# Optimization experiments

Hardware: AMD Instinct MI355X
Metric: run time of the kernel (lower is better)

The kernel has to match this reference:

```python
import jax, jax.numpy as jnp
import numpy as np

H = 400           # size_hidden_layer
F = 128           # nFeatures
S = 128           # seq_len
B = 256           # batch
K_OUT = 5         # size_output_layer


def lstm_layer(x, kernel, bias):
    """TF LSTMCell semantics: gates i, j, f, o; forget_bias=1.0.
    x: [B,S,D], kernel: [D+H, 4H], bias: [4H] -> returns [B,S,H]."""
    b = x.shape[0]
    h0 = jnp.zeros((b, H), x.dtype)
    c0 = jnp.zeros((b, H), x.dtype)
    xT = jnp.swapaxes(x, 0, 1)  # [S,B,D]

    def step(carry, xt):
        h, c = carry
        z = jnp.concatenate([xt, h], axis=1) @ kernel + bias  # [B,4H]
        i, j, f, o = jnp.split(z, 4, axis=1)
        c_new = c * jax.nn.sigmoid(f + 1.0) + jax.nn.sigmoid(i) * jnp.tanh(j)
        h_new = jnp.tanh(c_new) * jax.nn.sigmoid(o)
        return (h_new, c_new), h_new

    _, ys = jax.lax.scan(step, (h0, c0), xT)
    return jnp.swapaxes(ys, 0, 1)  # [B,S,H]


def setup_inputs() -> dict:
    key = jax.random.key(0)
    ks = jax.random.split(key, 8)
    x = jax.random.normal(ks[0], (B, S, F), dtype=jnp.float32)
    # LSTM kernels (glorot-ish small init); layer 0 input F, others H
    k0 = 0.05 * jax.random.normal(ks[1], (F + H, 4 * H), dtype=jnp.float32)
    k1 = 0.05 * jax.random.normal(ks[2], (H + H, 4 * H), dtype=jnp.float32)
    k2 = 0.05 * jax.random.normal(ks[3], (H + H, 4 * H), dtype=jnp.float32)
    b0 = jnp.zeros((4 * H,), jnp.float32)
    b1 = jnp.zeros((4 * H,), jnp.float32)
    b2 = jnp.zeros((4 * H,), jnp.float32)
    # Output heads: truncated_normal(stddev=0.01) weights, 0.1 biases
    w_lg = 0.01 * jax.random.normal(ks[4], (H, 1), dtype=jnp.float32)
    b_lg = jnp.full((1,), 0.1, jnp.float32)
    w_sm2 = 0.01 * jax.random.normal(ks[5], (H, 2), dtype=jnp.float32)
    b_sm2 = jnp.full((2,), 0.1, jnp.float32)
    w = 0.01 * jax.random.normal(ks[6], (H, K_OUT), dtype=jnp.float32)
    b = jnp.full((K_OUT,), 0.1, jnp.float32)
    return {"x": x, "k0": k0, "b0": b0, "k1": k1, "b1": b1, "k2": k2,
            "b2": b2, "w_lg": w_lg, "b_lg": b_lg, "w_sm2": w_sm2,
            "b_sm2": b_sm2, "w": w, "b": b}


def reference(x, k0, b0, k1, b1, k2, b2, w_lg, b_lg, w_sm2, b_sm2, w, b):
    h = lstm_layer(x, k0, b0)
    h = lstm_layer(h, k1, b1)
    h = lstm_layer(h, k2, b2)          # [B,S,H]
    pred_mc = jax.nn.sigmoid(h @ w_lg + b_lg)            # [B,S,1]
    pred_md = jax.nn.softmax(h @ w_sm2 + b_sm2, axis=-1)  # [B,S,2]
    pred_mg = jax.nn.softmax(h @ w + b, axis=-1)          # [B,S,5]
    return jnp.concatenate([pred_mc, pred_md, pred_mg], axis=-1)  # [B,S,8]
```

## Files before the change

kernel.cpp:

```cpp
#include <hip/hip_runtime.h>
#include <hip/hip_bf16.h>


typedef __attribute__((ext_vector_type(8))) short bf16x8;
typedef __attribute__((ext_vector_type(4))) float f32x4;

#define S_LEN 128
#define HID   400
#define NCOL  1600
#define NCB   25
#define KT_REC 13
#define WS_NEEDED 173358080ull

__device__ __forceinline__ f32x4 mfma16(bf16x8 a, bf16x8 b, f32x4 c) {
  return __builtin_amdgcn_mfma_f32_16x16x32_bf16(a, b, c, 0, 0, 0);
}
__device__ __forceinline__ void gll16(const void* g, void* l) {
  __builtin_amdgcn_global_load_lds(
      (const __attribute__((address_space(1))) void*)g,
      (__attribute__((address_space(3))) void*)l, 16, 0, 0);
}
__device__ __forceinline__ float bf2f(__hip_bfloat16 h) { return __bfloat162float(h); }
__device__ __forceinline__ __hip_bfloat16 f2bf(float f) { return __float2bfloat16(f); }
__device__ __forceinline__ float sigm(float x) { return 1.f / (1.f + __expf(-x)); }
__device__ __forceinline__ float tanh_fast(float x) { return 1.f - 2.f / (__expf(2.f * x) + 1.f); }

__global__ __launch_bounds__(256) void cvt_x_kernel(const float* __restrict__ x,
                                                    __hip_bfloat16* __restrict__ xbf) {
  const int i = blockIdx.x * 256 + threadIdx.x;
  float4 v = ((const float4*)x)[i];
  ushort4 u;
  u.x = __builtin_bit_cast(unsigned short, f2bf(v.x));
  u.y = __builtin_bit_cast(unsigned short, f2bf(v.y));
  u.z = __builtin_bit_cast(unsigned short, f2bf(v.z));
  u.w = __builtin_bit_cast(unsigned short, f2bf(v.w));
  ((ushort4*)xbf)[i] = u;
}

__global__ __launch_bounds__(256) void prep_gemm_frag(
    const float* __restrict__ K0, const float* __restrict__ K1,
    const float* __restrict__ K2, __hip_bfloat16* __restrict__ wfrag) {
  const int total = 3200 * 512;
  for (int e = blockIdx.x * 256 + threadIdx.x; e < total; e += gridDim.x * 256) {
    const int ch = e >> 9, r = e & 511;
    const int c16 = r & 15, j = (r >> 4) & 7, kg = r >> 7;
    const float* W; int Kv, chL;
    if (ch < 400)       { W = K0; Kv = 128; chL = ch; }
    else if (ch < 1800) { W = K1; Kv = 400; chL = ch - 400; }
    else                { W = K2; Kv = 400; chL = ch - 1800; }
    const int kt = chL / 100, nt = chL - kt * 100;
    const int k = kt * 32 + kg * 8 + j;
    const float v = (k < Kv) ? W[(long)k * NCOL + nt * 16 + c16] : 0.f;
    wfrag[(ch << 9) + ((kg * 16 + c16) << 3) + j] = f2bf(v);
  }
}

__global__ __launch_bounds__(256) void prep_rec_frag(
    const float* __restrict__ K0, const float* __restrict__ K1,
    const float* __restrict__ K2, __hip_bfloat16* __restrict__ rfrag) {
  const int perL = 25 * 52 * 512;
  const int total = 3 * perL;
  for (int e = blockIdx.x * 256 + threadIdx.x; e < total; e += gridDim.x * 256) {
    const int l = e / perL, eL = e - l * perL;
    const int ch = eL >> 9, r = eL & 511;
    const int c16 = r & 15, j = (r >> 4) & 7, kg = r >> 7;
    const int cb = ch / 52, rem = ch - cb * 52;
    const int kt = rem >> 2, w = rem & 3;
    const int k = kt * 32 + kg * 8 + j;
    const int col = w * 400 + cb * 16 + c16;
    const float* W = (l == 0) ? K0 : ((l == 1) ? K1 : K2);
    const int D = (l == 0) ? 128 : 400;
    const float v = (k < HID) ? W[(long)(D + k) * NCOL + col] : 0.f;
    rfrag[(long)l * perL + (ch << 9) + ((kg * 16 + c16) << 3) + j] = f2bf(v);
  }
}

__global__ __launch_bounds__(256) void gemm_kernel(
    const __hip_bfloat16* __restrict__ A, int lda, int kIters,
    const __hip_bfloat16* __restrict__ wfrag, const float* __restrict__ bias,
    __hip_bfloat16* __restrict__ C) {
  __shared__ uint4 lds4[32 * 64];
  char* lds = (char*)lds4;
  const int tid = threadIdx.x;
  const int wave = tid >> 6, lane = tid & 63;
  const int wm = wave >> 1, wn = wave & 1;
  const int m0 = blockIdx.x << 7, n0 = blockIdx.y << 7;

  f32x4 acc[4][4];
#pragma unroll
  for (int i = 0; i < 4; ++i)
#pragma unroll
    for (int j = 0; j < 4; ++j) acc[i][j] = (f32x4){0.f, 0.f, 0.f, 0.f};

  for (int it = 0; it < kIters; ++it) {
    const int k0 = it << 6;
#pragma unroll
    for (int q = 0; q < 8; ++q) {
      const int id = wave * 8 + q;
      char* dst = lds + (id << 10);
      if (id < 16) {
        const int kk = id >> 3, mt = id & 7;
        const int m = m0 + mt * 16 + (lane & 15);
        int k = k0 + kk * 32 + ((lane >> 4) << 3);
        if (k + 8 > lda) k = 0;
        gll16((const char*)A + (((long)m * lda + k) << 1), dst);
      } else {
        const int kk = (id >> 3) & 1, nt = id & 7;
        const int ktg = (it << 1) + kk;
        int ntg = (n0 >> 4) + nt;
        if (ntg > 99) ntg = 99;
        gll16((const char*)wfrag + ((((ktg * 100 + ntg) << 6) + lane) << 4), dst);
      }
    }
    asm volatile("s_waitcnt vmcnt(0)" ::: "memory");
    __syncthreads();
#pragma unroll
    for (int kk = 0; kk < 2; ++kk) {
      bf16x8 af[4], bfr[4];
#pragma unroll
      for (int i = 0; i < 4; ++i) {
        af[i]  = *(const bf16x8*)(lds + ((kk * 8 + wm * 4 + i) << 10) + (lane << 4));
        bfr[i] = *(const bf16x8*)(lds + ((16 + kk * 8 + wn * 4 + i) << 10) + (lane << 4));
      }
#pragma unroll
      for (int i = 0; i < 4; ++i)
#pragma unroll
        for (int j = 0; j < 4; ++j) acc[i][j] = mfma16(af[i], bfr[j], acc[i][j]);
    }
    __syncthreads();
  }
  const int rowbase = m0 + wm * 64 + ((lane >> 4) << 2);
  const int colbase = n0 + wn * 64 + (lane & 15);
#pragma unroll
  for (int j = 0; j < 4; ++j) {
    const int col = colbase + j * 16;
    if (col < NCOL) {
      const float bs = bias[col];
#pragma unroll
      for (int i = 0; i < 4; ++i) {
        const int row = rowbase + i * 16;
#pragma unroll
        for (int r = 0; r < 4; ++r)
          C[(long)(row + r) * NCOL + col] = f2bf(acc[i][j][r] + bs);
      }
    }
  }
}

__global__ __launch_bounds__(256) void rec_kernel(
    const __hip_bfloat16* __restrict__ rfrag,
    const __hip_bfloat16* __restrict__ preZ,
    __hip_bfloat16* __restrict__ Hout,
    __hip_bfloat16* __restrict__ hbuf,
    unsigned* __restrict__ flags) {
  __shared__ uint4 AldsV[26 * 64];
  __shared__ float zlds[4 * 32 * 16];
  char* Alds = (char*)AldsV;

  const int g = blockIdx.x & 7;
  const int cB = blockIdx.x >> 3;
  const int tid = threadIdx.x;
  const int wave = tid >> 6, lane = tid & 63;

  bf16x8 breg[KT_REC];
#pragma unroll
  for (int kt = 0; kt < KT_REC; ++kt) {
    uint4 u = ((const uint4*)rfrag)[((cB * KT_REC + kt) * 4 + wave) * 64 + lane];
    breg[kt] = __builtin_bit_cast(bf16x8, u);
  }

  float cst0 = 0.f, cst1 = 0.f;
  const int u16 = tid & 15, r0 = tid >> 4;

  for (int t = 0; t < S_LEN; ++t) {
    const int p = t & 1;

    const int b0r = g * 32 + r0;
    const long pz0 = ((long)b0r * S_LEN + t) * NCOL + cB * 16 + u16;
    const long pz1 = ((long)(b0r + 16) * S_LEN + t) * NCOL + cB * 16 + u16;
    const float pzi0 = bf2f(preZ[pz0]);
    const float pzj0 = bf2f(preZ[pz0 + 400]);
    const float pzf0 = bf2f(preZ[pz0 + 800]);
    const float pzo0 = bf2f(preZ[pz0 + 1200]);
    const float pzi1 = bf2f(preZ[pz1]);
    const float pzj1 = bf2f(preZ[pz1 + 400]);
    const float pzf1 = bf2f(preZ[pz1 + 800]);
    const float pzo1 = bf2f(preZ[pz1 + 1200]);

    for (int cc = wave; cc < 26; cc += 4) {
      const int kt = cc >> 1, mt = cc & 1;
      const int b = g * 32 + mt * 16 + (lane & 15);
      int k = kt * 32 + ((lane >> 4) << 3);
      if (k >= HID) k = 0;
      gll16((const char*)hbuf + (((p * 256 + b) * HID + k) << 1), Alds + (cc << 10));
    }
    asm volatile("s_waitcnt vmcnt(0)" ::: "memory");
    __syncthreads();

    f32x4 acc0 = (f32x4){0.f, 0.f, 0.f, 0.f}, acc1 = acc0;
#pragma unroll
    for (int kt = 0; kt < KT_REC; ++kt) {
      bf16x8 a0 = *(const bf16x8*)(Alds + ((kt * 2 + 0) << 10) + (lane << 4));
      bf16x8 a1 = *(const bf16x8*)(Alds + ((kt * 2 + 1) << 10) + (lane << 4));
      acc0 = mfma16(a0, breg[kt], acc0);
      acc1 = mfma16(a1, breg[kt], acc1);
    }
    {
      const int colz = lane & 15, rb = (lane >> 4) << 2;
#pragma unroll
      for (int r = 0; r < 4; ++r) {
        zlds[(wave * 32 + rb + r) * 16 + colz] = acc0[r];
        zlds[(wave * 32 + rb + r + 16) * 16 + colz] = acc1[r];
      }
    }
    __syncthreads();

#pragma unroll
    for (int half = 0; half < 2; ++half) {
      const int row = r0 + half * 16;
      const int b = g * 32 + row;
      const long mrow = (long)b * S_LEN + t;
      const float zi = zlds[(0 * 32 + row) * 16 + u16] + (half ? pzi1 : pzi0);
      const float zj = zlds[(1 * 32 + row) * 16 + u16] + (half ? pzj1 : pzj0);
      const float zf = zlds[(2 * 32 + row) * 16 + u16] + (half ? pzf1 : pzf0) + 1.f;
      const float zo = zlds[(3 * 32 + row) * 16 + u16] + (half ? pzo1 : pzo0);
      float c_old = half ? cst1 : cst0;
      const float cn = c_old * sigm(zf) + sigm(zi) * tanh_fast(zj);
      if (half) cst1 = cn; else cst0 = cn;
      const float hv = tanh_fast(cn) * sigm(zo);
      const __hip_bfloat16 hb16 = f2bf(hv);
      Hout[mrow * HID + cB * 16 + u16] = hb16;
      hbuf[((1 - p) * 256 + b) * HID + cB * 16 + u16] = hb16;
    }
    __threadfence();
    __syncthreads();
    if (t == S_LEN - 1) break;

    const unsigned tgt = (unsigned)(t + 1);
    if (tid == 0)
      __hip_atomic_store(&flags[g * 32 + cB], tgt, __ATOMIC_RELEASE,
                         __HIP_MEMORY_SCOPE_AGENT);
    if (wave == 0) {
      while (true) {
        unsigned v = tgt;
        if (lane < NCB)
          v = __hip_atomic_load(&flags[g * 32 + lane], __ATOMIC_ACQUIRE,
                                __HIP_MEMORY_SCOPE_AGENT);
        if (__all((int)(v >= tgt))) break;
        __builtin_amdgcn_s_sleep(2);
      }
    }
    __syncthreads();
    __threadfence();
  }
}

__global__ __launch_bounds__(256) void heads_kernel(
    const __hip_bfloat16* __restrict__ H, const float* __restrict__ wlg,
    const float* __restrict__ blg, const float* __restrict__ wsm2,
    const float* __restrict__ bsm2, const float* __restrict__ w5,
    const float* __restrict__ b5, float* __restrict__ out) {
  __shared__ float wc[8][400];
  const int tid = threadIdx.x;
  for (int e = tid; e < 3200; e += 256) {
    const int cc = e / 400, k = e - cc * 400;
    float v;
    if (cc == 0) v = wlg[k];
    else if (cc <= 2) v = wsm2[k * 2 + (cc - 1)];
    else v = w5[k * 5 + (cc - 3)];
    wc[cc][k] = v;
  }
  __syncthreads();
  const int wave = tid >> 6, lane = tid & 63;
  const int row = blockIdx.x * 4 + wave;
  const __hip_bfloat16* hrow = H + (long)row * HID;
  float pacc[8] = {0.f, 0.f, 0.f, 0.f, 0.f, 0.f, 0.f, 0.f};
  for (int k = lane; k < HID; k += 64) {
    const float hv = bf2f(hrow[k]);
#pragma unroll
    for (int cc = 0; cc < 8; ++cc) pacc[cc] += hv * wc[cc][k];
  }
#pragma unroll
  for (int cc = 0; cc < 8; ++cc)
    for (int off = 32; off > 0; off >>= 1)
      pacc[cc] += __shfl_xor(pacc[cc], off, 64);
  if (lane == 0) {
    const float o0 = sigm(pacc[0] + blg[0]);
    const float z1 = pacc[1] + bsm2[0], z2 = pacc[2] + bsm2[1];
    const float mm = fmaxf(z1, z2);
    const float e1 = __expf(z1 - mm), e2 = __expf(z2 - mm);
    const float inv2 = 1.f / (e1 + e2);
    float z5[5], m5 = -1e30f;
#pragma unroll
    for (int c = 0; c < 5; ++c) { z5[c] = pacc[3 + c] + b5[c]; m5 = fmaxf(m5, z5[c]); }
    float es[5], s5 = 0.f;
#pragma unroll
    for (int c = 0; c < 5; ++c) { es[c] = __expf(z5[c] - m5); s5 += es[c]; }
    const float inv5 = 1.f / s5;
    float4* op = (float4*)(out + (long)row * 8);
    op[0] = make_float4(o0, e1 * inv2, e2 * inv2, es[0] * inv5);
    op[1] = make_float4(es[1] * inv5, es[2] * inv5, es[3] * inv5, es[4] * inv5);
  }
}

extern "C" void kernel_launch(void* const* d_in, const int* in_sizes, int n_in,
                              void* d_out, int out_size, void* d_ws, size_t ws_size,
                              hipStream_t stream) {
  (void)in_sizes; (void)n_in; (void)out_size;
  if (ws_size < WS_NEEDED) return;

  const float* x    = (const float*)d_in[0];
  const float* K0   = (const float*)d_in[1];
  const float* B0   = (const float*)d_in[2];
  const float* K1   = (const float*)d_in[3];
  const float* B1   = (const float*)d_in[4];
  const float* K2   = (const float*)d_in[5];
  const float* B2   = (const float*)d_in[6];
  const float* wlg  = (const float*)d_in[7];
  const float* blg  = (const float*)d_in[8];
  const float* wsm2 = (const float*)d_in[9];
  const float* bsm2 = (const float*)d_in[10];
  const float* w5   = (const float*)d_in[11];
  const float* b5   = (const float*)d_in[12];
  float* out = (float*)d_out;
  char* ws = (char*)d_ws;

  __hip_bfloat16* xbf   = (__hip_bfloat16*)(ws + 0);
  __hip_bfloat16* HA    = (__hip_bfloat16*)(ws + 8388608);
  __hip_bfloat16* HB    = (__hip_bfloat16*)(ws + 34603008);
  __hip_bfloat16* preZ  = (__hip_bfloat16*)(ws + 60817408);
  __hip_bfloat16* hbuf  = (__hip_bfloat16*)(ws + 165675008);
  __hip_bfloat16* wfrag = (__hip_bfloat16*)(ws + 166084608);
  __hip_bfloat16* rfrag = (__hip_bfloat16*)(ws + 169361408);
  unsigned* flags       = (unsigned*)(ws + 173355008);

  hipMemsetAsync(flags, 0, 3072, stream);
  hipMemsetAsync(hbuf, 0, 204800, stream);
  cvt_x_kernel<<<4096, 256, 0, stream>>>(x, xbf);
  prep_gemm_frag<<<2048, 256, 0, stream>>>(K0, K1, K2, wfrag);
  prep_rec_frag<<<2048, 256, 0, stream>>>(K0, K1, K2, rfrag);

  gemm_kernel<<<dim3(256, 13), 256, 0, stream>>>(xbf, 128, 2, wfrag, B0, preZ);
  rec_kernel<<<200, 256, 0, stream>>>(rfrag, preZ, HA, hbuf, flags);

  hipMemsetAsync(hbuf, 0, 204800, stream);
  gemm_kernel<<<dim3(256, 13), 256, 0, stream>>>(HA, 400, 7, wfrag + 204800, B1, preZ);
  rec_kernel<<<200, 256, 0, stream>>>(rfrag + 665600, preZ, HB, hbuf, flags + 256);

  hipMemsetAsync(hbuf, 0, 204800, stream);
  gemm_kernel<<<dim3(256, 13), 256, 0, stream>>>(HB, 400, 7, wfrag + 921600, B2, preZ);
  rec_kernel<<<200, 256, 0, stream>>>(rfrag + 1331200, preZ, HA, hbuf, flags + 512);

  heads_kernel<<<8192, 256, 0, stream>>>(HA, wlg, blg, wsm2, bsm2, w5, b5, out);
}
```

Measured before the change: 13.43 ms.

## Replace multi-block flag-synced recurrence with per-batch-group single-block LSTM kernel

The recurrent step now runs as 16 independent blocks of 832 threads, each owning 16 batch rows and all 400 hidden units. This removes the cross-block atomic flag barriers and global h exchange. Recurrent weights are held in registers across 13 waves, h is ping-ponged in LDS, and next-step preZ is prefetched into LDS with async global-to-LDS loads. The cost is that only 16 CUs are used, with a very high register load per wave, so each block carries much more serial MFMA work per step.

```diff
diff --git a/kernel.cpp b/kernel.cpp
--- a/kernel.cpp
+++ b/kernel.cpp
@@ -8,9 +8,7 @@
 #define S_LEN 128
 #define HID   400
 #define NCOL  1600
-#define NCB   25
-#define KT_REC 13
-#define WS_NEEDED 173358080ull
+#define WS_NEEDED 173105152ull
 
 __device__ __forceinline__ f32x4 mfma16(bf16x8 a, bf16x8 b, f32x4 c) {
   return __builtin_amdgcn_mfma_f32_16x16x32_bf16(a, b, c, 0, 0, 0);
@@ -24,6 +22,10 @@
 __device__ __forceinline__ __hip_bfloat16 f2bf(float f) { return __float2bfloat16(f); }
 __device__ __forceinline__ float sigm(float x) { return 1.f / (1.f + __expf(-x)); }
 __device__ __forceinline__ float tanh_fast(float x) { return 1.f - 2.f / (__expf(2.f * x) + 1.f); }
+__device__ __forceinline__ float ldbf(const char* p) {
+  const unsigned short u = *(const unsigned short*)p;
+  return __builtin_bit_cast(float, (unsigned)u << 16);
+}
 
 __global__ __launch_bounds__(256) void cvt_x_kernel(const float* __restrict__ x,
                                                     __hip_bfloat16* __restrict__ xbf) {
@@ -58,20 +60,22 @@
 __global__ __launch_bounds__(256) void prep_rec_frag(
     const float* __restrict__ K0, const float* __restrict__ K1,
     const float* __restrict__ K2, __hip_bfloat16* __restrict__ rfrag) {
-  const int perL = 25 * 52 * 512;
+  const int perL = 1352 * 512;
   const int total = 3 * perL;
   for (int e = blockIdx.x * 256 + threadIdx.x; e < total; e += gridDim.x * 256) {
     const int l = e / perL, eL = e - l * perL;
     const int ch = eL >> 9, r = eL & 511;
-    const int c16 = r & 15, j = (r >> 4) & 7, kg = r >> 7;
-    const int cb = ch / 52, rem = ch - cb * 52;
-    const int kt = rem >> 2, w = rem & 3;
-    const int k = kt * 32 + kg * 8 + j;
-    const int col = w * 400 + cb * 16 + c16;
+    const int lane = r >> 3, j = r & 7;
+    const int kt = ch % 13;
+    int c2 = ch / 13;
+    const int ut = c2 & 1; c2 >>= 1;
+    const int q = c2 & 3;  const int w = c2 >> 2;
+    const int unit = w * 32 + ut * 16 + (lane & 15);
+    const int k = kt * 32 + ((lane >> 4) << 3) + j;
     const float* W = (l == 0) ? K0 : ((l == 1) ? K1 : K2);
     const int D = (l == 0) ? 128 : 400;
-    const float v = (k < HID) ? W[(long)(D + k) * NCOL + col] : 0.f;
-    rfrag[(long)l * perL + (ch << 9) + ((kg * 16 + c16) << 3) + j] = f2bf(v);
+    const float v = (k < HID && unit < HID) ? W[(long)(D + k) * NCOL + q * 400 + unit] : 0.f;
+    rfrag[(long)l * perL + (ch << 9) + (lane << 3) + j] = f2bf(v);
   }
 }
 
@@ -147,111 +151,120 @@
   }
 }
 
-__global__ __launch_bounds__(256) void rec_kernel(
-    const __hip_bfloat16* __restrict__ rfrag,
+__device__ __forceinline__ void stage_pz(const __hip_bfloat16* __restrict__ preZ,
+                                         int G, int t, char* dstbase,
+                                         int tid, int wv) {
+#pragma unroll
+  for (int it = 0; it < 4; ++it) {
+    const int s = it * 832 + tid;
+    if (s < 3200) {
+      const int row = s / 200;
+      const int off = s - row * 200;
+      const long gb = ((long)((G * 16 + row) * 128 + t)) * 3200 + (long)off * 16;
+      gll16((const char*)preZ + gb, dstbase + (it * 832 + (wv << 6)) * 16);
+    }
+  }
+}
+
+__global__ __launch_bounds__(832, 1) void rec2_kernel(
+    const __hip_bfloat16* __restrict__ rfragL,
     const __hip_bfloat16* __restrict__ preZ,
-    __hip_bfloat16* __restrict__ Hout,
-    __hip_bfloat16* __restrict__ hbuf,
-    unsigned* __restrict__ flags) {
-  __shared__ uint4 AldsV[26 * 64];
-  __shared__ float zlds[4 * 32 * 16];
-  char* Alds = (char*)AldsV;
-
-  const int g = blockIdx.x & 7;
-  const int cB = blockIdx.x >> 3;
+    __hip_bfloat16* __restrict__ Hout) {
+  __shared__ __attribute__((aligned(16))) char smem[129536];
+  char* const pz0 = smem;
+  char* const pz1 = smem + 51200;
+  char* const h0  = smem + 102400;
+  char* const h1  = smem + 102400 + 13568;
+
   const int tid = threadIdx.x;
-  const int wave = tid >> 6, lane = tid & 63;
-
-  bf16x8 breg[KT_REC];
-#pragma unroll
-  for (int kt = 0; kt < KT_REC; ++kt) {
-    uint4 u = ((const uint4*)rfrag)[((cB * KT_REC + kt) * 4 + wave) * 64 + lane];
-    breg[kt] = __builtin_bit_cast(bf16x8, u);
-  }
-
-  float cst0 = 0.f, cst1 = 0.f;
-  const int u16 = tid & 15, r0 = tid >> 4;
+  const int wv = tid >> 6, lane = tid & 63;
+  const int l15 = lane & 15, l4 = lane >> 4;
+  const int G = blockIdx.x;
+
+  for (int s = tid; s < 6784; s += 832) ((unsigned*)h0)[s] = 0;
+
+  stage_pz(preZ, G, 0, pz0, tid, wv);
+
+  bf16x8 Bw[4][2][13];
+  {
+    const uint4* rp = (const uint4*)rfragL;
+#pragma unroll
+    for (int q = 0; q < 4; ++q)
+#pragma unroll
+      for (int ut = 0; ut < 2; ++ut)
+#pragma unroll
+        for (int kt = 0; kt < 13; ++kt)
+          Bw[q][ut][kt] = __builtin_bit_cast(
+              bf16x8, rp[((((wv * 4 + q) * 2 + ut) * 13) + kt) * 64 + lane]);
+  }
+
+  float cs[2][4];
+#pragma unroll
+  for (int ut = 0; ut < 2; ++ut)
+#pragma unroll
+    for (int r = 0; r < 4; ++r) cs[ut][r] = 0.f;
+
+  const int hrow = l15 * 424 * 2;
+  __syncthreads();
 
   for (int t = 0; t < S_LEN; ++t) {
     const int p = t & 1;
-
-    const int b0r = g * 32 + r0;
-    const long pz0 = ((long)b0r * S_LEN + t) * NCOL + cB * 16 + u16;
-    const long pz1 = ((long)(b0r + 16) * S_LEN + t) * NCOL + cB * 16 + u16;
-    const float pzi0 = bf2f(preZ[pz0]);
-    const float pzj0 = bf2f(preZ[pz0 + 400]);
-    const float pzf0 = bf2f(preZ[pz0 + 800]);
-    const float pzo0 = bf2f(preZ[pz0 + 1200]);
-    const float pzi1 = bf2f(preZ[pz1]);
-    const float pzj1 = bf2f(preZ[pz1 + 400]);
-    const float pzf1 = bf2f(preZ[pz1 + 800]);
-    const float pzo1 = bf2f(preZ[pz1 + 1200]);
-
-    for (int cc = wave; cc < 26; cc += 4) {
-      const int kt = cc >> 1, mt = cc & 1;
-      const int b = g * 32 + mt * 16 + (lane & 15);
-      int k = kt * 32 + ((lane >> 4) << 3);
-      if (k >= HID) k = 0;
-      gll16((const char*)hbuf + (((p * 256 + b) * HID + k) << 1), Alds + (cc << 10));
-    }
-    asm volatile("s_waitcnt vmcnt(0)" ::: "memory");
+    if (t + 1 < S_LEN) stage_pz(preZ, G, t + 1, p ? pz0 : pz1, tid, wv);
+
+    const char* hc = p ? h1 : h0;
+    f32x4 acc[4][2];
+#pragma unroll
+    for (int q = 0; q < 4; ++q) {
+      acc[q][0] = (f32x4){0.f, 0.f, 0.f, 0.f};
+      acc[q][1] = (f32x4){0.f, 0.f, 0.f, 0.f};
+    }
+    if (wv < 12) {
+#pragma unroll
+      for (int kt = 0; kt < 13; ++kt) {
+        const bf16x8 a = *(const bf16x8*)(hc + hrow + ((kt * 32 + (l4 << 3)) << 1));
+#pragma unroll
+        for (int q = 0; q < 4; ++q) {
+          acc[q][0] = mfma16(a, Bw[q][0][kt], acc[q][0]);
+          acc[q][1] = mfma16(a, Bw[q][1][kt], acc[q][1]);
+        }
+      }
+    } else {
+#pragma unroll
+      for (int kt = 0; kt < 13; ++kt) {
+        const bf16x8 a = *(const bf16x8*)(hc + hrow + ((kt * 32 + (l4 << 3)) << 1));
+#pragma unroll
+        for (int q = 0; q < 4; ++q)
+          acc[q][0] = mfma16(a, Bw[q][0][kt], acc[q][0]);
+      }
+    }
+
+    const char* pzc = p ? pz1 : pz0;
+    char* hn = p ? h0 : h1;
+    const int tOff = t * 400;
+#define GATE_UT(UT)                                                           \
+    {                                                                         \
+      const int unit = wv * 32 + (UT)*16 + l15;                               \
+      _Pragma("unroll")                                                       \
+      for (int r = 0; r < 4; ++r) {                                           \
+        const int row = l4 * 4 + r;                                           \
+        const char* pzp = pzc + row * 3200 + unit * 2;                        \
+        const float zi = acc[0][UT][r] + ldbf(pzp);                           \
+        const float zj = acc[1][UT][r] + ldbf(pzp + 800);                     \
+        const float zf = acc[2][UT][r] + ldbf(pzp + 1600) + 1.f;              \
+        const float zo = acc[3][UT][r] + ldbf(pzp + 2400);                    \
+        const float cn = cs[UT][r] * sigm(zf) + sigm(zi) * tanh_fast(zj);     \
+        cs[UT][r] = cn;                                                       \
+        const float hv = tanh_fast(cn) * sigm(zo);                            \
+        const unsigned short hb = __builtin_bit_cast(unsigned short, f2bf(hv)); \
+        *(unsigned short*)(hn + ((row * 424 + unit) << 1)) = hb;              \
+        Hout[(long)G * 819200 + row * 51200 + tOff + unit] =                  \
+            __builtin_bit_cast(__hip_bfloat16, hb);                           \
+      }                                                                       \
+    }
+    GATE_UT(0)
+    if (wv < 12) GATE_UT(1)
+#undef GATE_UT
     __syncthreads();
-
-    f32x4 acc0 = (f32x4){0.f, 0.f, 0.f, 0.f}, acc1 = acc0;
-#pragma unroll
-    for (int kt = 0; kt < KT_REC; ++kt) {
-      bf16x8 a0 = *(const bf16x8*)(Alds + ((kt * 2 + 0) << 10) + (lane << 4));
-      bf16x8 a1 = *(const bf16x8*)(Alds + ((kt * 2 + 1) << 10) + (lane << 4));
-      acc0 = mfma16(a0, breg[kt], acc0);
-      acc1 = mfma16(a1, breg[kt], acc1);
-    }
-    {
-      const int colz = lane & 15, rb = (lane >> 4) << 2;
-#pragma unroll
-      for (int r = 0; r < 4; ++r) {
-        zlds[(wave * 32 + rb + r) * 16 + colz] = acc0[r];
-        zlds[(wave * 32 + rb + r + 16) * 16 + colz] = acc1[r];
-      }
-    }
-    __syncthreads();
-
-#pragma unroll
-    for (int half = 0; half < 2; ++half) {
-      const int row = r0 + half * 16;
-      const int b = g * 32 + row;
-      const long mrow = (long)b * S_LEN + t;
-      const float zi = zlds[(0 * 32 + row) * 16 + u16] + (half ? pzi1 : pzi0);
-      const float zj = zlds[(1 * 32 + row) * 16 + u16] + (half ? pzj1 : pzj0);
-      const float zf = zlds[(2 * 32 + row) * 16 + u16] + (half ? pzf1 : pzf0) + 1.f;
-      const float zo = zlds[(3 * 32 + row) * 16 + u16] + (half ? pzo1 : pzo0);
-      float c_old = half ? cst1 : cst0;
-      const float cn = c_old * sigm(zf) + sigm(zi) * tanh_fast(zj);
-      if (half) cst1 = cn; else cst0 = cn;
-      const float hv = tanh_fast(cn) * sigm(zo);
-      const __hip_bfloat16 hb16 = f2bf(hv);
-      Hout[mrow * HID + cB * 16 + u16] = hb16;
-      hbuf[((1 - p) * 256 + b) * HID + cB * 16 + u16] = hb16;
-    }
-    __threadfence();
-    __syncthreads();
-    if (t == S_LEN - 1) break;
-
-    const unsigned tgt = (unsigned)(t + 1);
-    if (tid == 0)
-      __hip_atomic_store(&flags[g * 32 + cB], tgt, __ATOMIC_RELEASE,
-                         __HIP_MEMORY_SCOPE_AGENT);
-    if (wave == 0) {
-      while (true) {
-        unsigned v = tgt;
-        if (lane < NCB)
-          v = __hip_atomic_load(&flags[g * 32 + lane], __ATOMIC_ACQUIRE,
-                                __HIP_MEMORY_SCOPE_AGENT);
-        if (__all((int)(v >= tgt))) break;
-        __builtin_amdgcn_s_sleep(2);
-      }
-    }
-    __syncthreads();
-    __threadfence();
   }
 }
 
@@ -329,27 +342,21 @@
   __hip_bfloat16* HA    = (__hip_bfloat16*)(ws + 8388608);
   __hip_bfloat16* HB    = (__hip_bfloat16*)(ws + 34603008);
   __hip_bfloat16* preZ  = (__hip_bfloat16*)(ws + 60817408);
-  __hip_bfloat16* hbuf  = (__hip_bfloat16*)(ws + 165675008);
-  __hip_bfloat16* wfrag = (__hip_bfloat16*)(ws + 166084608);
-  __hip_bfloat16* rfrag = (__hip_bfloat16*)(ws + 169361408);
-  unsigned* flags       = (unsigned*)(ws + 173355008);
-
-  hipMemsetAsync(flags, 0, 3072, stream);
-  hipMemsetAsync(hbuf, 0, 204800, stream);
+  __hip_bfloat16* wfrag = (__hip_bfloat16*)(ws + 165675008);
+  __hip_bfloat16* rfrag = (__hip_bfloat16*)(ws + 168951808);
+
   cvt_x_kernel<<<4096, 256, 0, stream>>>(x, xbf);
   prep_gemm_frag<<<2048, 256, 0, stream>>>(K0, K1, K2, wfrag);
   prep_rec_frag<<<2048, 256, 0, stream>>>(K0, K1, K2, rfrag);
 
   gemm_kernel<<<dim3(256, 13), 256, 0, stream>>>(xbf, 128, 2, wfrag, B0, preZ);
-  rec_kernel<<<200, 256, 0, stream>>>(rfrag, preZ, HA, hbuf, flags);
-
-  hipMemsetAsync(hbuf, 0, 204800, stream);
+  rec2_kernel<<<16, 832, 0, stream>>>(rfrag, preZ, HA);
+
   gemm_kernel<<<dim3(256, 13), 256, 0, stream>>>(HA, 400, 7, wfrag + 204800, B1, preZ);
-  rec_kernel<<<200, 256, 0, stream>>>(rfrag + 665600, preZ, HB, hbuf, flags + 256);
-
-  hipMemsetAsync(hbuf, 0, 204800, stream);
+  rec2_kernel<<<16, 832, 0, stream>>>(rfrag + 692224, preZ, HB);
+
   gemm_kernel<<<dim3(256, 13), 256, 0, stream>>>(HB, 400, 7, wfrag + 921600, B2, preZ);
-  rec_kernel<<<200, 256, 0, stream>>>(rfrag + 1331200, preZ, HA, hbuf, flags + 512);
+  rec2_kernel<<<16, 832, 0, stream>>>(rfrag + 1384448, preZ, HA);
 
   heads_kernel<<<8192, 256, 0, stream>>>(HA, wlg, blg, wsm2, bsm2, w5, b5, out);
 }
```

New measurement: 13.91 ms. 1.04x slower.
